# Performance work log

Measured on AMD Instinct MI355X. Metric: run time of the kernel, lower is better.

## Reference

```python
import jax, jax.numpy as jnp
import numpy as np

F_IN, H, D, C, NCLS = 1024, 512, 256, 10, 4


def setup_inputs() -> dict:
    key = jax.random.key(0)
    ks = jax.random.split(key, 20)
    N = 32768
    x_path = jax.random.normal(ks[0], (N, F_IN), dtype=jnp.float32)
    cluster_id = jax.random.randint(ks[1], (N,), 0, C, dtype=jnp.int64)
    s1 = 1.0 / np.sqrt(F_IN)
    s2 = 1.0 / np.sqrt(H)
    s3 = 1.0 / np.sqrt(D)
    return {
        "x_path": x_path,
        "cluster_id": cluster_id,
        "W1": jax.random.normal(ks[2], (C, F_IN, H), dtype=jnp.float32) * s1,
        "b1": jnp.zeros((C, H), dtype=jnp.float32),
        "W2": jax.random.normal(ks[3], (C, H, H), dtype=jnp.float32) * s2,
        "b2": jnp.zeros((C, H), dtype=jnp.float32),
        "fc_W": jax.random.normal(ks[4], (H, H), dtype=jnp.float32) * s2,
        "fc_b": jnp.zeros((H,), dtype=jnp.float32),
        "a_W": jax.random.normal(ks[5], (H, D), dtype=jnp.float32) * s2,
        "a_b": jnp.zeros((D,), dtype=jnp.float32),
        "g_W": jax.random.normal(ks[6], (H, D), dtype=jnp.float32) * s2,
        "g_b": jnp.zeros((D,), dtype=jnp.float32),
        "c_W": jax.random.normal(ks[7], (D, 1), dtype=jnp.float32) * s3,
        "c_b": jnp.zeros((1,), dtype=jnp.float32),
        "rho_W": jax.random.normal(ks[8], (H, D), dtype=jnp.float32) * s2,
        "rho_b": jnp.zeros((D,), dtype=jnp.float32),
        "cls_W": jax.random.normal(ks[9], (D, NCLS), dtype=jnp.float32) * s3,
        "cls_b": jnp.zeros((NCLS,), dtype=jnp.float32),
    }


def reference(x_path, cluster_id, W1, b1, W2, b2, fc_W, fc_b, a_W, a_b,
              g_W, g_b, c_W, c_b, rho_W, rho_b, cls_W, cls_b):
    relu = jax.nn.relu
    means = []
    for i in range(C):  # fixed small set of clusters (structurally distinct MLPs)
        m = (cluster_id == i).astype(x_path.dtype)          # [N]
        y = relu(relu(x_path @ W1[i] + b1[i]) @ W2[i] + b2[i])  # [N, H]
        cnt = jnp.maximum(m.sum(), 1.0)
        means.append((y * m[:, None]).sum(axis=0) / cnt)    # [H] segment mean
    h_cluster = jnp.stack(means, axis=0)                    # [C, H]
    h = relu(h_cluster @ fc_W + fc_b)                       # [C, H]
    a = jnp.tanh(h @ a_W + a_b)                             # [C, D]
    g = jax.nn.sigmoid(h @ g_W + g_b)                       # [C, D]
    A = (a * g) @ c_W + c_b                                 # [C, 1]
    A = jax.nn.softmax(A.T, axis=1)                         # [1, C]
    h_path = A @ h                                          # [1, H]
    h_path = relu(h_path @ rho_W + rho_b).squeeze()         # [D]
    logits = (h_path @ cls_W + cls_b)[None, :]              # [1, NCLS]
    Y_hat = jnp.argmax(logits, axis=1, keepdims=True)       # [1, 1]
    hazards = jax.nn.sigmoid(logits)
    S = jnp.cumprod(1.0 - hazards, axis=1)
    return hazards, S, Y_hat
```

## Files before the change

### kernel.cpp

```cpp
#include <hip/hip_runtime.h>
#include <hip/hip_fp16.h>
#include <math.h>

#define FIN 1024
#define H 512
#define DD 256
#define NCLS 4
#define MAXC 64

#define TMM 32
#define WCOLS 40

#define WS_TOFF 1088
#define WS_NZ   1408
#define WS_SUMS 1536

typedef _Float16 f16x8 __attribute__((ext_vector_type(8)));
typedef _Float16 f16x4 __attribute__((ext_vector_type(4)));
typedef _Float16 f16x2 __attribute__((ext_vector_type(2)));
typedef float    f32x4 __attribute__((ext_vector_type(4)));

__global__ void detect_kernel(const int* __restrict__ cid32, int* flag, int n) {
    int i = blockIdx.x * blockDim.x + threadIdx.x;
    bool p = (i < n) && (i & 1) && (cid32[i] != 0);
    unsigned long long m = __ballot(p);
    if (p && ((threadIdx.x & 63) == (__ffsll(m) - 1))) atomicOr(flag, 1);
}

__device__ __forceinline__ int get_cid(const int* cid, int flag, int i) {
    return flag ? cid[i] : cid[2 * i];
}

__global__ void count_kernel(const int* __restrict__ cid, const int* __restrict__ flag,
                             int* counts, int n, int C) {
    __shared__ int lc[MAXC];
    int tid = threadIdx.x;
    if (tid < C) lc[tid] = 0;
    __syncthreads();
    int i = blockIdx.x * blockDim.x + tid;
    if (i < n) {
        int c = get_cid(cid, *flag, i);
        if ((unsigned)c < (unsigned)C) atomicAdd(&lc[c], 1);
    }
    __syncthreads();
    if (tid < C && lc[tid] > 0) atomicAdd(&counts[tid], lc[tid]);
}

__global__ void offsets_kernel(const int* __restrict__ counts, int* offs, int* toff,
                               int C, int tilesz) {
    if (threadIdx.x == 0 && blockIdx.x == 0) {
        int s = 0, ts = 0;
        offs[0] = 0; toff[0] = 0;
        for (int c = 0; c < C; c++) {
            s += counts[c];                          offs[c + 1] = s;
            ts += (counts[c] + tilesz - 1) / tilesz; toff[c + 1] = ts;
        }
    }
}

__global__ void compact_kernel(const int* __restrict__ cid, const int* __restrict__ flag,
                               const int* __restrict__ offs, int* cursor,
                               int* lists, int n, int C) {
    __shared__ int lc[MAXC], lbase[MAXC], lpos[MAXC];
    int tid = threadIdx.x;
    if (tid < C) { lc[tid] = 0; lpos[tid] = 0; }
    __syncthreads();
    int i = blockIdx.x * blockDim.x + tid;
    int c = -1;
    if (i < n) {
        int cc = get_cid(cid, *flag, i);
        if ((unsigned)cc < (unsigned)C) { c = cc; atomicAdd(&lc[c], 1); }
    }
    __syncthreads();
    if (tid < C && lc[tid] > 0) lbase[tid] = atomicAdd(&cursor[tid], lc[tid]);
    __syncthreads();
    if (c >= 0) {
        int p = atomicAdd(&lpos[c], 1);
        lists[offs[c] + lbase[c] + p] = i;
    }
}


__device__ __forceinline__ int frag_off(int r, int g) {
    int blk = r >> 1;
    int slot = (((r & 1) << 2) | g) ^ (blk & 7);
    return blk * 128 + slot * 16;
}

__device__ __forceinline__ void gload1k(const char* g, char* l) {
    __builtin_amdgcn_global_load_lds(
        (const __attribute__((address_space(1))) void*)g,
        (__attribute__((address_space(3))) void*)l, 16, 0, 0);
}

__global__ __launch_bounds__(256) void wprep_kernel(
    const float* __restrict__ W, _Float16* __restrict__ hi,
    _Float16* __restrict__ lo, int K, int C)
{
    int ktn = K >> 5;
    int b = blockIdx.x;
    int c = b / (4 * ktn);
    int rem = b % (4 * ktn);
    int nb = rem / ktn, kt = rem % ktn;
    __shared__ float sw[32][132];
    const float* Wc = W + (size_t)c * K * H + (size_t)(kt * 32) * H + nb * 128;
    int tid = threadIdx.x;
#pragma unroll
    for (int it = 0; it < 4; it++) {
        int id = it * 256 + tid;
        int r = id >> 5, c4 = (id & 31) * 4;
        *(float4*)&sw[r][c4] = *(const float4*)(Wc + (size_t)r * H + c4);
    }
    __syncthreads();
    size_t tile = ((size_t)(c * 4 + nb)) * ktn + kt;
    char* hp = (char*)hi + tile * 8192;
    char* lp = (char*)lo + tile * 8192;
#pragma unroll
    for (int it = 0; it < 2; it++) {
        int fi = it * 256 + tid;
        int cl = fi >> 2, g = fi & 3;
        f16x8 hv, lv;
#pragma unroll
        for (int e = 0; e < 8; e++) {
            float v = sw[g * 8 + e][cl];
            _Float16 h = (_Float16)v;
            hv[e] = h;
            lv[e] = (_Float16)(v - (float)h);
        }
        int off = frag_off(cl, g);
        *(f16x8*)(hp + off) = hv;
        *(f16x8*)(lp + off) = lv;
    }
}

struct __align__(16) GSmem {
    union {
        struct { _Float16 A[4096]; _Float16 Bh[4096]; _Float16 Bl[4096]; } s;
        _Float16 Ct[128][132];
    } u;
    int sIdx[128];
};

__global__ __launch_bounds__(256) void gemm1(
    const float* __restrict__ x,
    const int* __restrict__ counts, const int* __restrict__ offs,
    const int* __restrict__ toff, const int* __restrict__ lists,
    const _Float16* __restrict__ wh, const _Float16* __restrict__ wl,
    const float* __restrict__ b1, _Float16* __restrict__ h1,
    int C, int nwg)
{
    int bid = blockIdx.x;
    {
        int q = nwg >> 3, r = nwg & 7, xcd = bid & 7, k = bid >> 3;
        bid = (xcd < r ? xcd * (q + 1) : r * (q + 1) + (xcd - r) * q) + k;
    }
    int ntile = toff[C];
    if (bid >= ntile * 4) return;
    int t = bid >> 2, nb = bid & 3;
    int c = 0;
    while (c + 1 < C && t >= toff[c + 1]) c++;
    int cnt = counts[c];
    int row0 = (t - toff[c]) * 128;

    __shared__ GSmem sm;
    int tid = threadIdx.x;
    int lane = tid & 63;
    int wave = __builtin_amdgcn_readfirstlane(tid >> 6);
    if (tid < 128) {
        int r = row0 + tid;
        sm.sIdx[tid] = (r < cnt) ? lists[offs[c] + r] : -1;
    }
    __syncthreads();

    int r0 = tid >> 2, g0 = tid & 3;
    int gi0 = sm.sIdx[r0], gi1 = sm.sIdx[64 + r0];
    const float* xp0 = x + (size_t)(gi0 < 0 ? 0 : gi0) * FIN + g0 * 8;
    const float* xp1 = x + (size_t)(gi1 < 0 ? 0 : gi1) * FIN + g0 * 8;
    int aoff0 = frag_off(r0, g0), aoff1 = frag_off(64 + r0, g0);

    const char* gh = (const char*)wh + ((size_t)(c * 4 + nb) * 32) * 8192;
    const char* gl = (const char*)wl + ((size_t)(c * 4 + nb) * 32) * 8192;
    char* ldsA  = (char*)sm.u.s.A;
    char* ldsBh = (char*)sm.u.s.Bh;
    char* ldsBl = (char*)sm.u.s.Bl;

    int wr = wave >> 1, wq = wave & 1;
    int l15 = lane & 15, g = lane >> 4;

    f32x4 acc[4][4];
#pragma unroll
    for (int i = 0; i < 4; i++)
#pragma unroll
        for (int j = 0; j < 4; j++) acc[i][j] = (f32x4){0.f, 0.f, 0.f, 0.f};

    for (int kt = 0; kt < 32; kt++) {
        __syncthreads();
        {
            int ch = wave * 2;
            const char* gsh = gh + (size_t)kt * 8192 + ch * 1024 + lane * 16;
            const char* gsl = gl + (size_t)kt * 8192 + ch * 1024 + lane * 16;
            gload1k(gsh,        ldsBh + ch * 1024);
            gload1k(gsh + 1024, ldsBh + ch * 1024 + 1024);
            gload1k(gsl,        ldsBl + ch * 1024);
            gload1k(gsl + 1024, ldsBl + ch * 1024 + 1024);
        }
        {
            float4 v0a = make_float4(0.f,0.f,0.f,0.f), v0b = v0a, v1a = v0a, v1b = v0a;
            if (gi0 >= 0) { v0a = *(const float4*)xp0; v0b = *(const float4*)(xp0 + 4); }
            if (gi1 >= 0) { v1a = *(const float4*)xp1; v1b = *(const float4*)(xp1 + 4); }
            f16x8 a0 = { (_Float16)v0a.x, (_Float16)v0a.y, (_Float16)v0a.z, (_Float16)v0a.w,
                         (_Float16)v0b.x, (_Float16)v0b.y, (_Float16)v0b.z, (_Float16)v0b.w };
            f16x8 a1 = { (_Float16)v1a.x, (_Float16)v1a.y, (_Float16)v1a.z, (_Float16)v1a.w,
                         (_Float16)v1b.x, (_Float16)v1b.y, (_Float16)v1b.z, (_Float16)v1b.w };
            *(f16x8*)(ldsA + aoff0) = a0;
            *(f16x8*)(ldsA + aoff1) = a1;
            xp0 += 32; xp1 += 32;
        }
        __syncthreads();
        f16x8 a[4], bh[4], bl[4];
#pragma unroll
        for (int fr = 0; fr < 4; fr++)
            a[fr] = *(const f16x8*)(ldsA + frag_off(wr * 64 + fr * 16 + l15, g));
#pragma unroll
        for (int fc = 0; fc < 4; fc++) {
            int col = wq * 64 + fc * 16 + l15;
            bh[fc] = *(const f16x8*)(ldsBh + frag_off(col, g));
            bl[fc] = *(const f16x8*)(ldsBl + frag_off(col, g));
        }
#pragma unroll
        for (int fr = 0; fr < 4; fr++)
#pragma unroll
            for (int fc = 0; fc < 4; fc++) {
                acc[fr][fc] = __builtin_amdgcn_mfma_f32_16x16x32_f16(a[fr], bh[fc], acc[fr][fc], 0, 0, 0);
                acc[fr][fc] = __builtin_amdgcn_mfma_f32_16x16x32_f16(a[fr], bl[fc], acc[fr][fc], 0, 0, 0);
            }
    }
    __syncthreads();
    const float* b1c = b1 + (size_t)c * H + nb * 128;
#pragma unroll
    for (int fc = 0; fc < 4; fc++) {
        int colL = wq * 64 + fc * 16 + l15;
        float bv = b1c[colL];
#pragma unroll
        for (int fr = 0; fr < 4; fr++)
#pragma unroll
            for (int j = 0; j < 4; j++) {
                int rowL = wr * 64 + fr * 16 + g * 4 + j;
                float v = acc[fr][fc][j] + bv;
                sm.u.Ct[rowL][colL] = (_Float16)(v > 0.f ? v : 0.f);
            }
    }
    __syncthreads();
    char* hout = (char*)h1 + ((size_t)t * 16 + nb * 4) * 8192;
#pragma unroll
    for (int ktl = 0; ktl < 4; ktl++)
#pragma unroll
        for (int it = 0; it < 2; it++) {
            int fi = it * 256 + tid;
            int rl = fi >> 2, gg = fi & 3;
            f16x8 v = *(const f16x8*)&sm.u.Ct[rl][ktl * 32 + gg * 8];
            *(f16x8*)(hout + (size_t)ktl * 8192 + frag_off(rl, gg)) = v;
        }
}

__global__ __launch_bounds__(256) void gemm2(
    const _Float16* __restrict__ h1,
    const int* __restrict__ counts, const int* __restrict__ toff,
    const _Float16* __restrict__ wh, const _Float16* __restrict__ wl,
    const float* __restrict__ b2, double* __restrict__ sums,
    int C, int nwg)
{
    int bid = blockIdx.x;
    {
        int q = nwg >> 3, r = nwg & 7, xcd = bid & 7, k = bid >> 3;
        bid = (xcd < r ? xcd * (q + 1) : r * (q + 1) + (xcd - r) * q) + k;
    }
    int ntile = toff[C];
    if (bid >= ntile * 4) return;
    int t = bid >> 2, nb = bid & 3;
    int c = 0;
    while (c + 1 < C && t >= toff[c + 1]) c++;
    int cnt = counts[c];
    int row0 = (t - toff[c]) * 128;

    __shared__ alignas(16) _Float16 sA2[4096];
    __shared__ alignas(16) _Float16 sBh2[4096];
    __shared__ alignas(16) _Float16 sBl2[4096];

    int tid = threadIdx.x;
    int lane = tid & 63;
    int wave = __builtin_amdgcn_readfirstlane(tid >> 6);
    int wr = wave >> 1, wq = wave & 1;
    int l15 = lane & 15, g = lane >> 4;

    const char* gA = (const char*)h1 + (size_t)t * 16 * 8192;
    const char* gh = (const char*)wh + ((size_t)(c * 4 + nb) * 16) * 8192;
    const char* gl = (const char*)wl + ((size_t)(c * 4 + nb) * 16) * 8192;

    f32x4 acc[4][4];
#pragma unroll
    for (int i = 0; i < 4; i++)
#pragma unroll
        for (int j = 0; j < 4; j++) acc[i][j] = (f32x4){0.f, 0.f, 0.f, 0.f};

    for (int kt = 0; kt < 16; kt++) {
        __syncthreads();
        int ch = wave * 2;
        const char* ga  = gA + (size_t)kt * 8192 + ch * 1024 + lane * 16;
        const char* gsh = gh + (size_t)kt * 8192 + ch * 1024 + lane * 16;
        const char* gsl = gl + (size_t)kt * 8192 + ch * 1024 + lane * 16;
        gload1k(ga,         (char*)sA2  + ch * 1024);
        gload1k(ga + 1024,  (char*)sA2  + ch * 1024 + 1024);
        gload1k(gsh,        (char*)sBh2 + ch * 1024);
        gload1k(gsh + 1024, (char*)sBh2 + ch * 1024 + 1024);
        gload1k(gsl,        (char*)sBl2 + ch * 1024);
        gload1k(gsl + 1024, (char*)sBl2 + ch * 1024 + 1024);
        __syncthreads();
        f16x8 a[4], bh[4], bl[4];
#pragma unroll
        for (int fr = 0; fr < 4; fr++)
            a[fr] = *(const f16x8*)((char*)sA2 + frag_off(wr * 64 + fr * 16 + l15, g));
#pragma unroll
        for (int fc = 0; fc < 4; fc++) {
            int col = wq * 64 + fc * 16 + l15;
            bh[fc] = *(const f16x8*)((char*)sBh2 + frag_off(col, g));
            bl[fc] = *(const f16x8*)((char*)sBl2 + frag_off(col, g));
        }
#pragma unroll
        for (int fr = 0; fr < 4; fr++)
#pragma unroll
            for (int fc = 0; fc < 4; fc++) {
                acc[fr][fc] = __builtin_amdgcn_mfma_f32_16x16x32_f16(a[fr], bh[fc], acc[fr][fc], 0, 0, 0);
                acc[fr][fc] = __builtin_amdgcn_mfma_f32_16x16x32_f16(a[fr], bl[fc], acc[fr][fc], 0, 0, 0);
            }
    }
    const float* b2c = b2 + (size_t)c * H + nb * 128;
    int rbound = cnt - row0;
    float psum[4];
#pragma unroll
    for (int fc = 0; fc < 4; fc++) {
        int colL = wq * 64 + fc * 16 + l15;
        float bv = b2c[colL];
        float s = 0.f;
#pragma unroll
        for (int fr = 0; fr < 4; fr++)
#pragma unroll
            for (int j = 0; j < 4; j++) {
                int rowL = wr * 64 + fr * 16 + g * 4 + j;
                float v = acc[fr][fc][j] + bv;
                v = v > 0.f ? v : 0.f;
                if (rowL < rbound) s += v;
            }
        psum[fc] = s;
    }
#pragma unroll
    for (int fc = 0; fc < 4; fc++) {
        psum[fc] += __shfl_xor(psum[fc], 16);
        psum[fc] += __shfl_xor(psum[fc], 32);
    }
    if (g == 0) {
#pragma unroll
        for (int fc = 0; fc < 4; fc++)
            atomicAdd(&sums[(size_t)c * H + nb * 128 + wq * 64 + fc * 16 + l15],
                      (double)psum[fc]);
    }
}

__global__ __launch_bounds__(256) void wsplit_kernel(
    const float* __restrict__ W, _Float16* __restrict__ hi,
    _Float16* __restrict__ lo, int K, int N)
{
    __shared__ float tile[64][65];
    int tid = threadIdx.x;
    int tilesN = N >> 6, tilesK = K >> 6;
    int b = blockIdx.x;
    int c = b / (tilesK * tilesN);
    int r = b % (tilesK * tilesN);
    int tk = r / tilesN, tn = r % tilesN;
    const float* Wc = W + (size_t)c * K * N;
    int k0 = tk << 6, n0 = tn << 6;
#pragma unroll
    for (int it = 0; it < 16; it++) {
        int id = it * 256 + tid;
        int kr = id >> 6, nc = id & 63;
        tile[kr][nc] = Wc[(size_t)(k0 + kr) * N + n0 + nc];
    }
    __syncthreads();
    _Float16* hic = hi + (size_t)c * N * K;
    _Float16* loc = lo + (size_t)c * N * K;
#pragma unroll
    for (int it = 0; it < 8; it++) {
        int id = it * 256 + tid;
        int nc = id >> 5, kp = (id & 31) * 2;
        float a0 = tile[kp][nc], a1 = tile[kp + 1][nc];
        _Float16 h0 = (_Float16)a0, h1v = (_Float16)a1;
        _Float16 l0 = (_Float16)(a0 - (float)h0);
        _Float16 l1 = (_Float16)(a1 - (float)h1v);
        size_t off = (size_t)(n0 + nc) * K + k0 + kp;
        f16x2 hv = {h0, h1v}, lv = {l0, l1};
        *(f16x2*)(hic + off) = hv;
        *(f16x2*)(loc + off) = lv;
    }
}

struct __align__(16) MfmaSmem {
    _Float16 sW[2][128][WCOLS];
    _Float16 sH[TMM][520];
    _Float16 sX[TMM][WCOLS];
    int      sIdx[TMM];
};

__global__ __launch_bounds__(256, 2) void mlp_mfma(
    const float* __restrict__ x,
    const int* __restrict__ counts, const int* __restrict__ offs,
    const int* __restrict__ toff, const int* __restrict__ lists,
    const _Float16* __restrict__ w1h, const _Float16* __restrict__ w1l,
    const _Float16* __restrict__ w2h, const _Float16* __restrict__ w2l,
    const float* __restrict__ b1, const float* __restrict__ b2,
    double* __restrict__ sums, int C, int nwg)
{
    int bid = blockIdx.x;
    {
        int q = nwg >> 3, r = nwg & 7, xcd = bid & 7, k = bid >> 3;
        bid = (xcd < r ? xcd * (q + 1) : r * (q + 1) + (xcd - r) * q) + k;
    }
    if (bid >= toff[C]) return;
    int c = 0;
    while (c + 1 < C && bid >= toff[c + 1]) c++;
    int t = bid - toff[c];
    int cnt = counts[c];
    int row0 = t * TMM;

    __shared__ MfmaSmem sm;
    int tid  = threadIdx.x;
    int lane = tid & 63, wave = tid >> 6;
    int wr = wave >> 1, wq = wave & 1;
    int l15 = lane & 15, g = lane >> 4;

    if (tid < TMM) {
        int r = row0 + tid;
        sm.sIdx[tid] = (r < cnt) ? lists[offs[c] + r] : -1;
    }

    const _Float16* w1hc = w1h + (size_t)c * FIN * H;
    const _Float16* w1lc = w1l + (size_t)c * FIN * H;
    const _Float16* w2hc = w2h + (size_t)c * H * H;
    const _Float16* w2lc = w2l + (size_t)c * H * H;
    const float* b1c = b1 + (size_t)c * H;
    const float* b2c = b2 + (size_t)c * H;

    int xr = tid >> 3;
    int xk = (tid & 7) * 4;
    int s_lc = tid >> 2;
    int s_kc = (tid & 3) * 8;

    for (int nb = 0; nb < H; nb += 128) {
        f32x4 acc[4];
#pragma unroll
        for (int f = 0; f < 4; f++) acc[f] = (f32x4){0.f, 0.f, 0.f, 0.f};

        for (int kk = 0; kk < FIN; kk += 32) {
            __syncthreads();
            {
                int gi = sm.sIdx[xr];
                float4 v = make_float4(0.f, 0.f, 0.f, 0.f);
                if (gi >= 0) v = *(const float4*)(x + (size_t)gi * FIN + kk + xk);
                f16x4 hv = { (_Float16)v.x, (_Float16)v.y, (_Float16)v.z, (_Float16)v.w };
                *(f16x4*)&sm.sX[xr][xk] = hv;
            }
            {
                const _Float16* ph = w1hc + (size_t)(nb + s_lc) * FIN + kk + s_kc;
                const _Float16* pl = w1lc + (size_t)(nb + s_lc) * FIN + kk + s_kc;
                *(f16x8*)&sm.sW[0][s_lc][s_kc]      = *(const f16x8*)ph;
                *(f16x8*)&sm.sW[0][64 + s_lc][s_kc] = *(const f16x8*)(ph + (size_t)64 * FIN);
                *(f16x8*)&sm.sW[1][s_lc][s_kc]      = *(const f16x8*)pl;
                *(f16x8*)&sm.sW[1][64 + s_lc][s_kc] = *(const f16x8*)(pl + (size_t)64 * FIN);
            }
            __syncthreads();
            f16x8 a = *(const f16x8*)&sm.sX[wr * 16 + l15][g * 8];
#pragma unroll
            for (int f = 0; f < 4; f++) {
                int lc = wq * 64 + f * 16 + l15;
                f16x8 bh = *(const f16x8*)&sm.sW[0][lc][g * 8];
                f16x8 bl = *(const f16x8*)&sm.sW[1][lc][g * 8];
                acc[f] = __builtin_amdgcn_mfma_f32_16x16x32_f16(a, bh, acc[f], 0, 0, 0);
                acc[f] = __builtin_amdgcn_mfma_f32_16x16x32_f16(a, bl, acc[f], 0, 0, 0);
            }
        }
#pragma unroll
        for (int f = 0; f < 4; f++) {
            int col = nb + wq * 64 + f * 16 + l15;
            float bv = b1c[col];
#pragma unroll
            for (int j = 0; j < 4; j++) {
                int row = wr * 16 + g * 4 + j;
                float v = acc[f][j] + bv;
                sm.sH[row][col] = (_Float16)(v > 0.f ? v : 0.f);
            }
        }
    }

    for (int nb = 0; nb < H; nb += 128) {
        f32x4 acc[4];
#pragma unroll
        for (int f = 0; f < 4; f++) acc[f] = (f32x4){0.f, 0.f, 0.f, 0.f};

        for (int kk = 0; kk < H; kk += 32) {
            __syncthreads();
            {
                const _Float16* ph = w2hc + (size_t)(nb + s_lc) * H + kk + s_kc;
                const _Float16* pl = w2lc + (size_t)(nb + s_lc) * H + kk + s_kc;
                *(f16x8*)&sm.sW[0][s_lc][s_kc]      = *(const f16x8*)ph;
                *(f16x8*)&sm.sW[0][64 + s_lc][s_kc] = *(const f16x8*)(ph + (size_t)64 * H);
                *(f16x8*)&sm.sW[1][s_lc][s_kc]      = *(const f16x8*)pl;
                *(f16x8*)&sm.sW[1][64 + s_lc][s_kc] = *(const f16x8*)(pl + (size_t)64 * H);
            }
            __syncthreads();
            f16x8 a = *(const f16x8*)&sm.sH[wr * 16 + l15][kk + g * 8];
#pragma unroll
            for (int f = 0; f < 4; f++) {
                int lc = wq * 64 + f * 16 + l15;
                f16x8 bh = *(const f16x8*)&sm.sW[0][lc][g * 8];
                f16x8 bl = *(const f16x8*)&sm.sW[1][lc][g * 8];
                acc[f] = __builtin_amdgcn_mfma_f32_16x16x32_f16(a, bh, acc[f], 0, 0, 0);
                acc[f] = __builtin_amdgcn_mfma_f32_16x16x32_f16(a, bl, acc[f], 0, 0, 0);
            }
        }
        float psum[4];
#pragma unroll
        for (int f = 0; f < 4; f++) {
            int col = nb + wq * 64 + f * 16 + l15;
            float bv = b2c[col];
            float s = 0.f;
#pragma unroll
            for (int j = 0; j < 4; j++) {
                int row = wr * 16 + g * 4 + j;
                float v = acc[f][j] + bv;
                v = v > 0.f ? v : 0.f;
                if (sm.sIdx[row] >= 0) s += v;
            }
            psum[f] = s;
        }
#pragma unroll
        for (int f = 0; f < 4; f++) {
            psum[f] += __shfl_xor(psum[f], 16);
            psum[f] += __shfl_xor(psum[f], 32);
        }
        if (g == 0) {
#pragma unroll
            for (int f = 0; f < 4; f++) {
                int col = nb + wq * 64 + f * 16 + l15;
                atomicAdd(&sums[(size_t)c * H + col], (double)psum[f]);
            }
        }
    }
}

__global__ __launch_bounds__(256) void row_mlp(
    const float* __restrict__ x, const int* __restrict__ cid,
    const int* __restrict__ flag,
    const float* __restrict__ W1, const float* __restrict__ b1,
    const float* __restrict__ W2, const float* __restrict__ b2,
    double* __restrict__ sums, int n, int C)
{
    int r = blockIdx.x;
    if (r >= n) return;
    int c = get_cid(cid, *flag, r);
    if ((unsigned)c >= (unsigned)C) return;

    __shared__ float sx[FIN];
    __shared__ float sh[H];
    int tid = threadIdx.x;

    for (int i = tid; i < FIN; i += 256) sx[i] = x[(size_t)r * FIN + i];
    __syncthreads();

    const float* W1c = W1 + (size_t)c * FIN * H;
    const float* b1c = b1 + (size_t)c * H;
    for (int col = tid; col < H; col += 256) {
        float acc = 0.f;
        for (int k = 0; k < FIN; k++) acc += sx[k] * W1c[(size_t)k * H + col];
        acc += b1c[col];
        sh[col] = acc > 0.f ? acc : 0.f;
    }
    __syncthreads();

    const float* W2c = W2 + (size_t)c * H * H;
    const float* b2c = b2 + (size_t)c * H;
    for (int col = tid; col < H; col += 256) {
        float acc = 0.f;
        for (int k = 0; k < H; k++) acc += sh[k] * W2c[(size_t)k * H + col];
        acc += b2c[col];
        float y = acc > 0.f ? acc : 0.f;
        atomicAdd(&sums[(size_t)c * H + col], (double)y);
    }
}

__global__ __launch_bounds__(128) void tailA_kernel(
    const int* __restrict__ counts, const double* __restrict__ sums,
    const float* __restrict__ fcW, const float* __restrict__ fcb,
    double* __restrict__ h_ws, int* __restrict__ nzflag)
{
    int b = blockIdx.x;
    int c = b >> 2, ch = b & 3;
    int tid = threadIdx.x;
    __shared__ double shc[H];
    double denom = fmax((double)counts[c], 1.0);
    double nz = 0.0;
    for (int i = tid; i < H; i += 128) {
        double v = sums[(size_t)c * H + i];
        nz += fabs(v);
        shc[i] = v / denom;
    }
    if (ch == 0) {
        if (__any(nz != 0.0) && (tid & 63) == 0) atomicOr(nzflag, 1);
    }
    __syncthreads();
    int col = ch * 128 + tid;
    double acc = 0.0;
#pragma unroll 16
    for (int k = 0; k < H; k++) acc += shc[k] * (double)fcW[k * H + col];
    acc += (double)fcb[col];
    h_ws[(size_t)c * H + col] = acc > 0.0 ? acc : 0.0;
}

__global__ __launch_bounds__(128) void tailB_kernel(
    const double* __restrict__ h_ws,
    const float* __restrict__ aW, const float* __restrict__ ab,
    const float* __restrict__ gW, const float* __restrict__ gb,
    double* __restrict__ ag_ws)
{
    int b = blockIdx.x;
    int c = b >> 1, dh = b & 1;
    int tid = threadIdx.x;
    __shared__ double sh[H];
    for (int i = tid; i < H; i += 128) sh[i] = h_ws[(size_t)c * H + i];
    __syncthreads();
    int d = dh * 128 + tid;
    double aa = (double)ab[d], gg = (double)gb[d];
#pragma unroll 8
    for (int k = 0; k < H; k++) {
        double hv = sh[k];
        aa += hv * (double)aW[k * DD + d];
        gg += hv * (double)gW[k * DD + d];
    }
    ag_ws[(size_t)c * DD + d] = tanh(aa) / (1.0 + exp(-gg));
}

__global__ __launch_bounds__(256) void tailC_kernel(
    const double* __restrict__ h_ws, const double* __restrict__ ag_ws,
    const float* __restrict__ cW, const float* __restrict__ cb,
    const float* __restrict__ rhoW, const float* __restrict__ rhob,
    const float* __restrict__ clsW, const float* __restrict__ clsb,
    const int* __restrict__ counts, const int* __restrict__ nzflag,
    const int* __restrict__ cid_raw, int n, int C,
    float* __restrict__ out)
{
    int tid = threadIdx.x;
    int lane = tid & 63, w = tid >> 6;
    __shared__ double sA[MAXC];
    __shared__ double shp[H];
    __shared__ double sr[DD];
    __shared__ double lgs[NCLS];

    for (int c = w; c < C; c += 4) {
        double acc = 0.0;
        for (int d = lane; d < DD; d += 64)
            acc += ag_ws[(size_t)c * DD + d] * (double)cW[d];
#pragma unroll
        for (int off = 32; off >= 1; off >>= 1) acc += __shfl_xor(acc, off);
        if (lane == 0) sA[c] = acc + (double)cb[0];
    }
    __syncthreads();
    if (tid == 0) {
        double m = sA[0];
        for (int c = 1; c < C; c++) m = fmax(m, sA[c]);
        double s = 0.0;
        for (int c = 0; c < C; c++) { sA[c] = exp(sA[c] - m); s += sA[c]; }
        for (int c = 0; c < C; c++) sA[c] /= s;
    }
    __syncthreads();
    for (int col = tid; col < H; col += 256) {
        double s = 0.0;
        for (int c = 0; c < C; c++) s += sA[c] * h_ws[(size_t)c * H + col];
        shp[col] = s;
    }
    __syncthreads();
    {
        int d = tid;
        double acc = 0.0;
#pragma unroll 16
        for (int k = 0; k < H; k++) acc += shp[k] * (double)rhoW[k * DD + d];
        acc += (double)rhob[d];
        sr[d] = acc > 0.0 ? acc : 0.0;
    }
    __syncthreads();
    for (int kk = w; kk < NCLS; kk += 4) {
        double acc = 0.0;
        for (int d = lane; d < DD; d += 64)
            acc += sr[d] * (double)clsW[d * NCLS + kk];
#pragma unroll
        for (int off = 32; off >= 1; off >>= 1) acc += __shfl_xor(acc, off);
        if (lane == 0) lgs[kk] = acc + (double)clsb[kk];
    }
    __syncthreads();
    if (tid == 0) {
        int am = 0;
        double best = lgs[0];
        double run = 1.0;
        for (int kk = 0; kk < NCLS; kk++) {
            if (lgs[kk] > best) { best = lgs[kk]; am = kk; }
            double hz = 1.0 / (1.0 + exp(-lgs[kk]));
            out[kk] = (float)hz;
            run *= (1.0 - hz);
            out[NCLS + kk] = (float)run;
        }
        long long cnt_total = 0;
        for (int c = 0; c < C; c++) cnt_total += counts[c];
        float yout;
        if (cnt_total == 0) {
            yout = 4.0e6f + (float)((cid_raw[0] & 0xFFF) + 4096 * (cid_raw[1] & 0xFFF));
        } else if (cnt_total != (long long)n) {
            yout = 2.0e6f + (float)cnt_total;
        } else if (*nzflag == 0) {
            yout = 3.0e6f;
        } else {
            yout = (float)am;
        }
        out[2 * NCLS] = yout;
    }
}

__global__ void diag_kernel(float* __restrict__ out, float code) {
    if (threadIdx.x == 0) {
        double run = 1.0;
        for (int kk = 0; kk < NCLS; kk++) {
            out[kk] = 0.5f;
            run *= 0.5;
            out[NCLS + kk] = (float)run;
        }
        out[2 * NCLS] = code;
    }
}

extern "C" void kernel_launch(void* const* d_in, const int* in_sizes, int n_in,
                              void* d_out, int out_size, void* d_ws, size_t ws_size,
                              hipStream_t stream) {
    const float* x    = (const float*)d_in[0];
    const int*   cid  = (const int*)d_in[1];
    const float* W1   = (const float*)d_in[2];
    const float* b1   = (const float*)d_in[3];
    const float* W2   = (const float*)d_in[4];
    const float* b2   = (const float*)d_in[5];
    const float* fcW  = (const float*)d_in[6];
    const float* fcb  = (const float*)d_in[7];
    const float* aW   = (const float*)d_in[8];
    const float* ab   = (const float*)d_in[9];
    const float* gW   = (const float*)d_in[10];
    const float* gb   = (const float*)d_in[11];
    const float* cW   = (const float*)d_in[12];
    const float* cb   = (const float*)d_in[13];
    const float* rhoW = (const float*)d_in[14];
    const float* rhob = (const float*)d_in[15];
    const float* clsW = (const float*)d_in[16];
    const float* clsb = (const float*)d_in[17];
    float* out = (float*)d_out;

    long long n = in_sizes[1];
    long long C = (in_sizes[7] > 0) ? (long long)in_sizes[3] / in_sizes[7] : 0;
    bool shapes_ok =
        n > 0 &&
        (long long)in_sizes[0] == n * FIN &&
        in_sizes[7] == H && in_sizes[9] == DD && in_sizes[17] == NCLS &&
        C >= 1 && C <= MAXC &&
        (long long)in_sizes[2] == C * FIN * H &&
        (long long)in_sizes[4] == C * H * H;

    size_t hws_off   = WS_SUMS + (size_t)C * H * 8;
    size_t agws_off  = hws_off + (size_t)C * H * 8;
    size_t lists_off = agws_off + (size_t)C * DD * 8;
    size_t wt_off    = (lists_off + (size_t)n * 4 + 255) & ~(size_t)255;
    size_t w1t_bytes = (size_t)C * H * FIN * 2;
    size_t w2t_bytes = (size_t)C * H * H * 2;
    size_t w1h_off   = wt_off;
    size_t w1l_off   = w1h_off + w1t_bytes;
    size_t w2h_off   = w1l_off + w1t_bytes;
    size_t w2l_off   = w2h_off + w2t_bytes;
    size_t h1_off    = (w2l_off + w2t_bytes + 255) & ~(size_t)255;
    int    nn = (int)n, CC = (int)C;
    int    ntile_ub  = (nn + 127) / 128 + CC;
    size_t h1_bytes  = (size_t)ntile_ub * 16 * 8192;
    size_t ws_full   = h1_off + h1_bytes;
    size_t ws_mid    = h1_off;
    size_t ws_row    = lists_off;

    if (!shapes_ok) {
        diag_kernel<<<1, 64, 0, stream>>>(out, 7.0e6f + (float)(C >= 0 ? C : 0));
        return;
    }
    if (ws_size < ws_row) {
        diag_kernel<<<1, 64, 0, stream>>>(
            out, 6.0e6f + (float)(ws_size > 0 ? (ws_size >> 10) : 0));
        return;
    }

    char* ws = (char*)d_ws;
    int*    counts = (int*)ws;
    int*    flag   = (int*)(ws + 256);
    int*    cursor = (int*)(ws + 512);
    int*    offs   = (int*)(ws + 768);
    int*    toff   = (int*)(ws + WS_TOFF);
    int*    nzflag = (int*)(ws + WS_NZ);
    double* sums   = (double*)(ws + WS_SUMS);
    double* h_ws   = (double*)(ws + hws_off);
    double* ag_ws  = (double*)(ws + agws_off);
    int*    lists  = (int*)(ws + lists_off);
    _Float16* w1h  = (_Float16*)(ws + w1h_off);
    _Float16* w1l  = (_Float16*)(ws + w1l_off);
    _Float16* w2h  = (_Float16*)(ws + w2h_off);
    _Float16* w2l  = (_Float16*)(ws + w2l_off);
    _Float16* h1   = (_Float16*)(ws + h1_off);

    int nb = (nn + 255) / 256;

    hipMemsetAsync(ws, 0, hws_off, stream);

    detect_kernel<<<nb, 256, 0, stream>>>(cid, flag, nn);
    count_kernel<<<nb, 256, 0, stream>>>(cid, flag, counts, nn, CC);

    if (ws_size >= ws_full) {
        offsets_kernel<<<1, 64, 0, stream>>>(counts, offs, toff, CC, 128);
        compact_kernel<<<nb, 256, 0, stream>>>(cid, flag, offs, cursor, lists, nn, CC);
        wprep_kernel<<<CC * 4 * (FIN / 32), 256, 0, stream>>>(W1, w1h, w1l, FIN, CC);
        wprep_kernel<<<CC * 4 * (H / 32), 256, 0, stream>>>(W2, w2h, w2l, H, CC);
        int grid = ntile_ub * 4;
        gemm1<<<grid, 256, 0, stream>>>(x, counts, offs, toff, lists,
                                        w1h, w1l, b1, h1, CC, grid);
        gemm2<<<grid, 256, 0, stream>>>(h1, counts, toff, w2h, w2l, b2,
                                        sums, CC, grid);
    } else if (ws_size >= ws_mid) {
        offsets_kernel<<<1, 64, 0, stream>>>(counts, offs, toff, CC, TMM);
        compact_kernel<<<nb, 256, 0, stream>>>(cid, flag, offs, cursor, lists, nn, CC);
        wsplit_kernel<<<CC * (FIN / 64) * (H / 64), 256, 0, stream>>>(W1, w1h, w1l, FIN, H);
        wsplit_kernel<<<CC * (H / 64) * (H / 64), 256, 0, stream>>>(W2, w2h, w2l, H, H);
        int nt = (nn + TMM - 1) / TMM + CC;
        mlp_mfma<<<nt, 256, 0, stream>>>(x, counts, offs, toff, lists,
                                         w1h, w1l, w2h, w2l, b1, b2,
                                         sums, CC, nt);
    } else {
        row_mlp<<<nn, 256, 0, stream>>>(x, cid, flag, W1, b1, W2, b2, sums, nn, CC);
    }

    tailA_kernel<<<CC * 4, 128, 0, stream>>>(counts, sums, fcW, fcb, h_ws, nzflag);
    tailB_kernel<<<CC * 2, 128, 0, stream>>>(h_ws, aW, ab, gW, gb, ag_ws);
    tailC_kernel<<<1, 256, 0, stream>>>(h_ws, ag_ws, cW, cb, rhoW, rhob,
                                        clsW, clsb, counts, nzflag, cid,
                                        nn, CC, out);
}
```

Before: 536.5 us.

## Double-buffer LDS tiles in both GEMMs and merge weight-prep launches

Both grouped GEMM kernels now use two LDS buffers for the A and B tiles. The next K-slice is prefetched (global-to-LDS loads plus the x fp32-to-fp16 conversion in gemm1) while MFMAs run on the current slice, which leaves one barrier per iteration instead of two. Launch bounds now request 3 waves per SIMD, and the two weight-split launches are merged into a single kernel. The cost is twice the LDS per block, which may limit occupancy, plus extra register pressure from holding the prefetched x values across the MFMA block.

```diff
diff --git a/kernel.cpp b/kernel.cpp
--- a/kernel.cpp
+++ b/kernel.cpp
@@ -93,18 +93,15 @@
         (__attribute__((address_space(3))) void*)l, 16, 0, 0);
 }
 
-__global__ __launch_bounds__(256) void wprep_kernel(
+__device__ __forceinline__ void wprep_body(
     const float* __restrict__ W, _Float16* __restrict__ hi,
-    _Float16* __restrict__ lo, int K, int C)
+    _Float16* __restrict__ lo, int K, int b, float sw[32][132], int tid)
 {
     int ktn = K >> 5;
-    int b = blockIdx.x;
     int c = b / (4 * ktn);
     int rem = b % (4 * ktn);
     int nb = rem / ktn, kt = rem % ktn;
-    __shared__ float sw[32][132];
     const float* Wc = W + (size_t)c * K * H + (size_t)(kt * 32) * H + nb * 128;
-    int tid = threadIdx.x;
 #pragma unroll
     for (int it = 0; it < 4; it++) {
         int id = it * 256 + tid;
@@ -133,15 +130,28 @@
     }
 }
 
+__global__ __launch_bounds__(256) void wprep_both(
+    const float* __restrict__ W1, _Float16* __restrict__ w1h, _Float16* __restrict__ w1l,
+    const float* __restrict__ W2, _Float16* __restrict__ w2h, _Float16* __restrict__ w2l,
+    int C)
+{
+    __shared__ float sw[32][132];
+    int n1 = C * 4 * (FIN / 32);
+    int b = blockIdx.x;
+    int tid = threadIdx.x;
+    if (b < n1) wprep_body(W1, w1h, w1l, FIN, b, sw, tid);
+    else        wprep_body(W2, w2h, w2l, H, b - n1, sw, tid);
+}
+
 struct __align__(16) GSmem {
     union {
-        struct { _Float16 A[4096]; _Float16 Bh[4096]; _Float16 Bl[4096]; } s;
+        struct { _Float16 A[2][4096]; _Float16 Bh[2][4096]; _Float16 Bl[2][4096]; } s;
         _Float16 Ct[128][132];
     } u;
     int sIdx[128];
 };
 
-__global__ __launch_bounds__(256) void gemm1(
+__global__ __launch_bounds__(256, 3) void gemm1(
     const float* __restrict__ x,
     const int* __restrict__ counts, const int* __restrict__ offs,
     const int* __restrict__ toff, const int* __restrict__ lists,
@@ -183,6 +193,7 @@
     char* ldsA  = (char*)sm.u.s.A;
     char* ldsBh = (char*)sm.u.s.Bh;
     char* ldsBl = (char*)sm.u.s.Bl;
+    int ch = wave * 2;
 
     int wr = wave >> 1, wq = wave & 1;
     int l15 = lane & 15, g = lane >> 4;
@@ -193,47 +204,69 @@
 #pragma unroll
         for (int j = 0; j < 4; j++) acc[i][j] = (f32x4){0.f, 0.f, 0.f, 0.f};
 
+    {
+        const char* gsh = gh + ch * 1024 + lane * 16;
+        const char* gsl = gl + ch * 1024 + lane * 16;
+        gload1k(gsh,        ldsBh + ch * 1024);
+        gload1k(gsh + 1024, ldsBh + ch * 1024 + 1024);
+        gload1k(gsl,        ldsBl + ch * 1024);
+        gload1k(gsl + 1024, ldsBl + ch * 1024 + 1024);
+        float4 v0a = make_float4(0.f,0.f,0.f,0.f), v0b = v0a, v1a = v0a, v1b = v0a;
+        if (gi0 >= 0) { v0a = *(const float4*)xp0; v0b = *(const float4*)(xp0 + 4); }
+        if (gi1 >= 0) { v1a = *(const float4*)xp1; v1b = *(const float4*)(xp1 + 4); }
+        f16x8 a0 = { (_Float16)v0a.x, (_Float16)v0a.y, (_Float16)v0a.z, (_Float16)v0a.w,
+                     (_Float16)v0b.x, (_Float16)v0b.y, (_Float16)v0b.z, (_Float16)v0b.w };
+        f16x8 a1 = { (_Float16)v1a.x, (_Float16)v1a.y, (_Float16)v1a.z, (_Float16)v1a.w,
+                     (_Float16)v1b.x, (_Float16)v1b.y, (_Float16)v1b.z, (_Float16)v1b.w };
+        *(f16x8*)(ldsA + aoff0) = a0;
+        *(f16x8*)(ldsA + aoff1) = a1;
+        xp0 += 32; xp1 += 32;
+    }
+    __syncthreads();
+
+    int cur = 0;
     for (int kt = 0; kt < 32; kt++) {
-        __syncthreads();
-        {
-            int ch = wave * 2;
-            const char* gsh = gh + (size_t)kt * 8192 + ch * 1024 + lane * 16;
-            const char* gsl = gl + (size_t)kt * 8192 + ch * 1024 + lane * 16;
-            gload1k(gsh,        ldsBh + ch * 1024);
-            gload1k(gsh + 1024, ldsBh + ch * 1024 + 1024);
-            gload1k(gsl,        ldsBl + ch * 1024);
-            gload1k(gsl + 1024, ldsBl + ch * 1024 + 1024);
-        }
-        {
-            float4 v0a = make_float4(0.f,0.f,0.f,0.f), v0b = v0a, v1a = v0a, v1b = v0a;
+        int nxt = cur ^ 1;
+        bool pf = kt < 31;
+        float4 v0a = make_float4(0.f,0.f,0.f,0.f), v0b = v0a, v1a = v0a, v1b = v0a;
+        if (pf) {
+            const char* gsh = gh + (size_t)(kt + 1) * 8192 + ch * 1024 + lane * 16;
+            const char* gsl = gl + (size_t)(kt + 1) * 8192 + ch * 1024 + lane * 16;
+            gload1k(gsh,        ldsBh + nxt * 8192 + ch * 1024);
+            gload1k(gsh + 1024, ldsBh + nxt * 8192 + ch * 1024 + 1024);
+            gload1k(gsl,        ldsBl + nxt * 8192 + ch * 1024);
+            gload1k(gsl + 1024, ldsBl + nxt * 8192 + ch * 1024 + 1024);
             if (gi0 >= 0) { v0a = *(const float4*)xp0; v0b = *(const float4*)(xp0 + 4); }
             if (gi1 >= 0) { v1a = *(const float4*)xp1; v1b = *(const float4*)(xp1 + 4); }
+            xp0 += 32; xp1 += 32;
+        }
+        f16x8 a[4], bh[4], bl[4];
+#pragma unroll
+        for (int fr = 0; fr < 4; fr++)
+            a[fr] = *(const f16x8*)(ldsA + cur * 8192 + frag_off(wr * 64 + fr * 16 + l15, g));
+#pragma unroll
+        for (int fc = 0; fc < 4; fc++) {
+            int col = wq * 64 + fc * 16 + l15;
+            bh[fc] = *(const f16x8*)(ldsBh + cur * 8192 + frag_off(col, g));
+            bl[fc] = *(const f16x8*)(ldsBl + cur * 8192 + frag_off(col, g));
+        }
+#pragma unroll
+        for (int fr = 0; fr < 4; fr++)
+#pragma unroll
+            for (int fc = 0; fc < 4; fc++) {
+                acc[fr][fc] = __builtin_amdgcn_mfma_f32_16x16x32_f16(a[fr], bh[fc], acc[fr][fc], 0, 0, 0);
+                acc[fr][fc] = __builtin_amdgcn_mfma_f32_16x16x32_f16(a[fr], bl[fc], acc[fr][fc], 0, 0, 0);
+            }
+        if (pf) {
             f16x8 a0 = { (_Float16)v0a.x, (_Float16)v0a.y, (_Float16)v0a.z, (_Float16)v0a.w,
                          (_Float16)v0b.x, (_Float16)v0b.y, (_Float16)v0b.z, (_Float16)v0b.w };
             f16x8 a1 = { (_Float16)v1a.x, (_Float16)v1a.y, (_Float16)v1a.z, (_Float16)v1a.w,
                          (_Float16)v1b.x, (_Float16)v1b.y, (_Float16)v1b.z, (_Float16)v1b.w };
-            *(f16x8*)(ldsA + aoff0) = a0;
-            *(f16x8*)(ldsA + aoff1) = a1;
-            xp0 += 32; xp1 += 32;
+            *(f16x8*)(ldsA + nxt * 8192 + aoff0) = a0;
+            *(f16x8*)(ldsA + nxt * 8192 + aoff1) = a1;
         }
         __syncthreads();
-        f16x8 a[4], bh[4], bl[4];
-#pragma unroll
-        for (int fr = 0; fr < 4; fr++)
-            a[fr] = *(const f16x8*)(ldsA + frag_off(wr * 64 + fr * 16 + l15, g));
-#pragma unroll
-        for (int fc = 0; fc < 4; fc++) {
-            int col = wq * 64 + fc * 16 + l15;
-            bh[fc] = *(const f16x8*)(ldsBh + frag_off(col, g));
-            bl[fc] = *(const f16x8*)(ldsBl + frag_off(col, g));
-        }
-#pragma unroll
-        for (int fr = 0; fr < 4; fr++)
-#pragma unroll
-            for (int fc = 0; fc < 4; fc++) {
-                acc[fr][fc] = __builtin_amdgcn_mfma_f32_16x16x32_f16(a[fr], bh[fc], acc[fr][fc], 0, 0, 0);
-                acc[fr][fc] = __builtin_amdgcn_mfma_f32_16x16x32_f16(a[fr], bl[fc], acc[fr][fc], 0, 0, 0);
-            }
+        cur = nxt;
     }
     __syncthreads();
     const float* b1c = b1 + (size_t)c * H + nb * 128;
@@ -263,7 +296,7 @@
         }
 }
 
-__global__ __launch_bounds__(256) void gemm2(
+__global__ __launch_bounds__(256, 3) void gemm2(
     const _Float16* __restrict__ h1,
     const int* __restrict__ counts, const int* __restrict__ toff,
     const _Float16* __restrict__ wh, const _Float16* __restrict__ wl,
@@ -283,15 +316,16 @@
     int cnt = counts[c];
     int row0 = (t - toff[c]) * 128;
 
-    __shared__ alignas(16) _Float16 sA2[4096];
-    __shared__ alignas(16) _Float16 sBh2[4096];
-    __shared__ alignas(16) _Float16 sBl2[4096];
+    __shared__ alignas(16) _Float16 sA2[2][4096];
+    __shared__ alignas(16) _Float16 sBh2[2][4096];
+    __shared__ alignas(16) _Float16 sBl2[2][4096];
 
     int tid = threadIdx.x;
     int lane = tid & 63;
     int wave = __builtin_amdgcn_readfirstlane(tid >> 6);
     int wr = wave >> 1, wq = wave & 1;
     int l15 = lane & 15, g = lane >> 4;
+    int ch = wave * 2;
 
     const char* gA = (const char*)h1 + (size_t)t * 16 * 8192;
     const char* gh = (const char*)wh + ((size_t)(c * 4 + nb) * 16) * 8192;
@@ -303,28 +337,42 @@
 #pragma unroll
         for (int j = 0; j < 4; j++) acc[i][j] = (f32x4){0.f, 0.f, 0.f, 0.f};
 
-    for (int kt = 0; kt < 16; kt++) {
-        __syncthreads();
-        int ch = wave * 2;
-        const char* ga  = gA + (size_t)kt * 8192 + ch * 1024 + lane * 16;
-        const char* gsh = gh + (size_t)kt * 8192 + ch * 1024 + lane * 16;
-        const char* gsl = gl + (size_t)kt * 8192 + ch * 1024 + lane * 16;
+    {
+        const char* ga  = gA + ch * 1024 + lane * 16;
+        const char* gsh = gh + ch * 1024 + lane * 16;
+        const char* gsl = gl + ch * 1024 + lane * 16;
         gload1k(ga,         (char*)sA2  + ch * 1024);
         gload1k(ga + 1024,  (char*)sA2  + ch * 1024 + 1024);
         gload1k(gsh,        (char*)sBh2 + ch * 1024);
         gload1k(gsh + 1024, (char*)sBh2 + ch * 1024 + 1024);
         gload1k(gsl,        (char*)sBl2 + ch * 1024);
         gload1k(gsl + 1024, (char*)sBl2 + ch * 1024 + 1024);
-        __syncthreads();
+    }
+    __syncthreads();
+
+    int cur = 0;
+    for (int kt = 0; kt < 16; kt++) {
+        int nxt = cur ^ 1;
+        if (kt < 15) {
+            const char* ga  = gA + (size_t)(kt + 1) * 8192 + ch * 1024 + lane * 16;
+            const char* gsh = gh + (size_t)(kt + 1) * 8192 + ch * 1024 + lane * 16;
+            const char* gsl = gl + (size_t)(kt + 1) * 8192 + ch * 1024 + lane * 16;
+            gload1k(ga,         (char*)sA2  + nxt * 8192 + ch * 1024);
+            gload1k(ga + 1024,  (char*)sA2  + nxt * 8192 + ch * 1024 + 1024);
+            gload1k(gsh,        (char*)sBh2 + nxt * 8192 + ch * 1024);
+            gload1k(gsh + 1024, (char*)sBh2 + nxt * 8192 + ch * 1024 + 1024);
+            gload1k(gsl,        (char*)sBl2 + nxt * 8192 + ch * 1024);
+            gload1k(gsl + 1024, (char*)sBl2 + nxt * 8192 + ch * 1024 + 1024);
+        }
         f16x8 a[4], bh[4], bl[4];
 #pragma unroll
         for (int fr = 0; fr < 4; fr++)
-            a[fr] = *(const f16x8*)((char*)sA2 + frag_off(wr * 64 + fr * 16 + l15, g));
+            a[fr] = *(const f16x8*)((char*)sA2 + cur * 8192 + frag_off(wr * 64 + fr * 16 + l15, g));
 #pragma unroll
         for (int fc = 0; fc < 4; fc++) {
             int col = wq * 64 + fc * 16 + l15;
-            bh[fc] = *(const f16x8*)((char*)sBh2 + frag_off(col, g));
-            bl[fc] = *(const f16x8*)((char*)sBl2 + frag_off(col, g));
+            bh[fc] = *(const f16x8*)((char*)sBh2 + cur * 8192 + frag_off(col, g));
+            bl[fc] = *(const f16x8*)((char*)sBl2 + cur * 8192 + frag_off(col, g));
         }
 #pragma unroll
         for (int fr = 0; fr < 4; fr++)
@@ -333,6 +381,8 @@
                 acc[fr][fc] = __builtin_amdgcn_mfma_f32_16x16x32_f16(a[fr], bh[fc], acc[fr][fc], 0, 0, 0);
                 acc[fr][fc] = __builtin_amdgcn_mfma_f32_16x16x32_f16(a[fr], bl[fc], acc[fr][fc], 0, 0, 0);
             }
+        __syncthreads();
+        cur = nxt;
     }
     const float* b2c = b2 + (size_t)c * H + nb * 128;
     int rbound = cnt - row0;
@@ -831,8 +881,8 @@
     if (ws_size >= ws_full) {
         offsets_kernel<<<1, 64, 0, stream>>>(counts, offs, toff, CC, 128);
         compact_kernel<<<nb, 256, 0, stream>>>(cid, flag, offs, cursor, lists, nn, CC);
-        wprep_kernel<<<CC * 4 * (FIN / 32), 256, 0, stream>>>(W1, w1h, w1l, FIN, CC);
-        wprep_kernel<<<CC * 4 * (H / 32), 256, 0, stream>>>(W2, w2h, w2l, H, CC);
+        wprep_both<<<CC * 4 * (FIN / 32 + H / 32), 256, 0, stream>>>(
+            W1, w1h, w1l, W2, w2h, w2l, CC);
         int grid = ntile_ub * 4;
         gemm1<<<grid, 256, 0, stream>>>(x, counts, offs, toff, lists,
                                         w1h, w1l, b1, h1, CC, grid);
```

Result: no change. 526.1 us (-1.9%).
